# Performance work log

Measured on AMD Instinct MI355X. Metric: run time of the kernel, lower is better.

The kernel has to match this reference:

```python
import jax, jax.numpy as jnp
import numpy as np

NQ = 4
NL = 3
HEADS = 8

_H = jnp.asarray(np.array([[1, 1], [1, -1]], np.complex64) / np.sqrt(2.0))
_X = jnp.asarray(np.array([[0, 1], [1, 0]], np.complex64))
_Y = jnp.asarray(np.array([[0, -1j], [1j, 0]], np.complex64))
_Z = jnp.asarray(np.array([[1, 0], [0, -1]], np.complex64))
_CNOT = jnp.asarray(np.array([[1, 0, 0, 0], [0, 1, 0, 0], [0, 0, 0, 1], [0, 0, 1, 0]], np.complex64))


def _rx(t):
    c = jnp.cos(t / 2).astype(jnp.complex64)
    s = (-1j * jnp.sin(t / 2)).astype(jnp.complex64)
    return jnp.stack([jnp.stack([c, s]), jnp.stack([s, c])])


def _ry(t):
    c = jnp.cos(t / 2).astype(jnp.complex64)
    s = jnp.sin(t / 2).astype(jnp.complex64)
    return jnp.stack([jnp.stack([c, -s]), jnp.stack([s, c])])


def _rz(t):
    e = jnp.exp((-0.5j) * t).astype(jnp.complex64)
    z = jnp.zeros((), jnp.complex64)
    return jnp.stack([jnp.stack([e, z]), jnp.stack([z, jnp.conj(e)])])


def _crx(t):
    # control-RX in |control,target> basis
    return jnp.eye(4, dtype=jnp.complex64).at[2:, 2:].set(_rx(t))


def _ap1(psi, U, q):
    # apply 2x2 gate U on qubit axis q of psi:(2,2,2,2)
    return jnp.moveaxis(jnp.tensordot(U, psi, axes=[[1], [q]]), 0, q)


def _ap2(psi, U, q1, q2):
    p = jnp.moveaxis(psi, (q1, q2), (0, 1)).reshape(4, 4)
    p = (U @ p).reshape(2, 2, 2, 2)
    return jnp.moveaxis(p, (0, 1), (q1, q2))


def _expv(psi, P, q):
    return jnp.real(jnp.vdot(psi, _ap1(psi, P, q)))


def _circuit(inp, w, ew, gam, bet):
    # inp:(4,)  w,ew:(3,4)  gam,bet:(3,)  -> (12,) expvals Z,X,Y
    psi = jnp.zeros((16,), jnp.complex64).at[0].set(1.0).reshape(2, 2, 2, 2)
    for i in range(NQ):  # AngleEmbedding(rotation='Y')
        psi = _ap1(psi, _ry(inp[i]), i)
    for L in range(NL):
        for i in range(NQ):
            psi = _ap1(psi, _rx(w[L, i]), i)
            psi = _ap1(psi, _ry(w[L, i]), i)
            psi = _ap1(psi, _rz(w[L, i]), i)
        for i in range(NQ):  # CRX entangling ring
            psi = _ap2(psi, _crx(ew[L, i]), i, (i + 1) % NQ)
        # Grover diffusion
        for q in range(NQ):
            psi = _ap1(psi, _H, q)
        for q in range(NQ):
            psi = _ap1(psi, _X, q)
        psi = _ap1(psi, _H, NQ - 1)
        psi = psi.at[1, 1, 1, :].set(psi[1, 1, 1, ::-1])  # CCCX ctrl=[0,1,2] tgt=3
        psi = _ap1(psi, _H, NQ - 1)
        for q in range(NQ):
            psi = _ap1(psi, _X, q)
        for q in range(NQ):
            psi = _ap1(psi, _H, q)
        # QAOA cost + mixer
        for i in range(NQ - 1):
            psi = _ap2(psi, _CNOT, i, i + 1)
            psi = _ap1(psi, _rz(gam[L]), i + 1)
            psi = _ap2(psi, _CNOT, i, i + 1)
        for q in range(NQ):
            psi = _ap1(psi, _rx(bet[L]), q)
    meas = [_expv(psi, _Z, q) for q in range(NQ)]
    meas += [_expv(psi, _X, q) for q in range(NQ)]
    meas += [_expv(psi, _Y, q) for q in range(NQ)]
    return jnp.stack(meas)


_vqc = jax.vmap(_circuit, in_axes=(0, None, None, None, None))


def _layernorm(x, g, b, eps=1e-5):
    mu = jnp.mean(x, -1, keepdims=True)
    var = jnp.mean((x - mu) ** 2, -1, keepdims=True)
    return (x - mu) * jax.lax.rsqrt(var + eps) * g + b


def _qtransform(xf, Wp, bp, ln_g, ln_b, w, ew, gam, bet):
    p = jnp.tanh(xf @ Wp.T + bp)  # (BS,4)
    p = _layernorm(p, ln_g, ln_b)
    return _vqc(p, w, ew, gam, bet)  # (BS,12)


def setup_inputs() -> dict:
    key = jax.random.key(0)
    ks = jax.random.split(key, 32)
    B, S, Hd = 4, 1024, 512
    d = {"x": jax.random.normal(ks[0], (B, S, Hd), jnp.float32)}
    d["Wp"] = jax.random.normal(ks[1], (NQ, Hd), jnp.float32) * 0.05
    d["bp"] = jnp.zeros((NQ,), jnp.float32)
    d["ln_g"] = jnp.ones((NQ,), jnp.float32)
    d["ln_b"] = jnp.zeros((NQ,), jnp.float32)
    i = 2
    for pfx in ["q", "k", "v"]:
        d[pfx + "w"] = 0.01 * jax.random.normal(ks[i], (NL, NQ), jnp.float32)
        d[pfx + "e"] = 0.01 * jax.random.normal(ks[i + 1], (NL, NQ), jnp.float32)
        d[pfx + "g"] = 0.01 * jax.random.normal(ks[i + 2], (NL,), jnp.float32)
        d[pfx + "b"] = 0.01 * jax.random.normal(ks[i + 3], (NL,), jnp.float32)
        i += 4
    fused = 3 * NQ
    d["Wq"] = jax.random.normal(ks[i], (Hd, fused), jnp.float32) * 0.2
    d["bq"] = jnp.zeros((Hd,), jnp.float32)
    d["Wk"] = jax.random.normal(ks[i + 1], (Hd, fused), jnp.float32) * 0.2
    d["bk"] = jnp.zeros((Hd,), jnp.float32)
    d["Wv"] = jax.random.normal(ks[i + 2], (Hd, fused), jnp.float32) * 0.2
    d["bv"] = jnp.zeros((Hd,), jnp.float32)
    d["Wo"] = jax.random.normal(ks[i + 3], (Hd, Hd), jnp.float32) * 0.05
    d["bo"] = jnp.zeros((Hd,), jnp.float32)
    return d


def reference(x, Wp, bp, ln_g, ln_b, qw, qe, qg, qb, kw, ke, kg, kb, vw, ve, vg, vb,
              Wq, bq, Wk, bk, Wv, bv, Wo, bo):
    B, S, Hd = x.shape
    hd = Hd // HEADS
    xf = x.reshape(B * S, Hd)
    tq = _qtransform(xf, Wp, bp, ln_g, ln_b, qw, qe, qg, qb)
    tk = _qtransform(xf, Wp, bp, ln_g, ln_b, kw, ke, kg, kb)
    tv = _qtransform(xf, Wp, bp, ln_g, ln_b, vw, ve, vg, vb)
    q = (tq @ Wq.T + bq).reshape(B, S, HEADS, hd)
    k = (tk @ Wk.T + bk).reshape(B, S, HEADS, hd)
    v = (tv @ Wv.T + bv).reshape(B, S, HEADS, hd)
    scale = float(hd) ** 0.5
    attn = jax.nn.softmax(jnp.einsum('bqhd,bkhd->bhqk', q, k) / scale, axis=-1)
    out = jnp.einsum('bhqk,bkhd->bqhd', attn, v).reshape(B, S, Hd)
    return out @ Wo.T + bo
```

## Files before the change

### kernel.cpp

```cpp
#include <hip/hip_runtime.h>
#include <hip/hip_bf16.h>
#include <math.h>

#define NROWS 4096
#define HD 512
#define HEADS 8
#define HDD 64
#define SEQ 1024
#define QSCALE 0.18033688011112042f

typedef unsigned short u16;
typedef unsigned int u32;
typedef __attribute__((ext_vector_type(8))) short sh8;
typedef __attribute__((ext_vector_type(4))) float f4;

__device__ __forceinline__ f4 mfma16(sh8 a, sh8 b, f4 c) {
  return __builtin_amdgcn_mfma_f32_16x16x32_bf16(a, b, c, 0, 0, 0);
}

__device__ __forceinline__ u16 f2bf(float x) {
  union { float f; unsigned u; } v; v.f = x;
  unsigned r = v.u + 0x7fff + ((v.u >> 16) & 1);
  return (u16)(r >> 16);
}

#define SWZA(r, cb) ((((r) * 128) + (cb)) ^ (((r) & 7) << 4))
#define SWZB(r, cb) ((((r) * 256) + (cb)) ^ (((r) & 7) << 4))

__global__ __launch_bounds__(256) void k_prep(
    const float* __restrict__ qw, const float* __restrict__ qe,
    const float* __restrict__ qg, const float* __restrict__ qb,
    const float* __restrict__ kw, const float* __restrict__ ke,
    const float* __restrict__ kg, const float* __restrict__ kb,
    const float* __restrict__ vw, const float* __restrict__ ve,
    const float* __restrict__ vg, const float* __restrict__ vb,
    const float* __restrict__ Wq, const float* __restrict__ bq,
    const float* __restrict__ Wk, const float* __restrict__ bk,
    const float* __restrict__ Wv, const float* __restrict__ bv,
    float* __restrict__ Mout, u16* __restrict__ Wbout) {
  const int c = blockIdx.x;
  const int tid = threadIdx.x;

  if (c >= 3) {
    const int c2 = c - 3;
    const float* W = (c2 == 0) ? Wq : (c2 == 1) ? Wk : Wv;
    const float* bb = (c2 == 0) ? bq : (c2 == 1) ? bk : bv;
    const float sc = (c2 == 0) ? QSCALE : 1.f;
    for (int o = tid; o < 512; o += 256) {
      unsigned out[16];
#pragma unroll
      for (int i = 0; i < 16; ++i) out[i] = 0u;
      const float* wr = W + o * 12;
#pragma unroll
      for (int jp = 0; jp < 6; ++jp)
        out[jp] = (unsigned)f2bf(wr[2*jp] * sc) | ((unsigned)f2bf(wr[2*jp+1] * sc) << 16);
      out[6] = (unsigned)f2bf(bb[o] * sc);
      unsigned* dst = (unsigned*)(Wbout + (c2 * 512 + o) * 32);
#pragma unroll
      for (int i = 0; i < 16; ++i) dst[i] = out[i];
    }
    return;
  }

  __shared__ float aC[32], aS[32];
  __shared__ float GT[60][8];
  __shared__ int   GM[60][2];
  __shared__ float PF[3][16][2];
  __shared__ float SR[16][17], SI[16][17];
  __shared__ float TS[16], TI[16];
  __shared__ float Ur[256], Ui[256];

  const float* w = (c == 0) ? qw : (c == 1) ? kw : vw;
  const float* e = (c == 0) ? qe : (c == 1) ? ke : ve;
  const float* g = (c == 0) ? qg : (c == 1) ? kg : vg;
  const float* b = (c == 0) ? qb : (c == 1) ? kb : vb;

  if (tid < 30) {
    float ang = (tid < 12) ? w[tid] : (tid < 24) ? e[tid - 12]
               : (tid < 27) ? g[tid - 24] : b[tid - 27];
    float s_, c_;
    sincosf(0.5f * ang, &s_, &c_);
    aC[tid] = c_; aS[tid] = s_;
  }
  __syncthreads();

  if (tid < 60) {
    int L = tid / 20, s5 = tid % 20;
    int typ, aidx, M, C;
    if (s5 < 12) {
      int q = s5 / 3; typ = s5 % 3; aidx = L * 4 + q; M = 8 >> q; C = 0;
    } else if (s5 < 16) {
      int q = s5 - 12; typ = 0; aidx = 12 + L * 4 + q;
      C = 8 >> q; M = 8 >> ((q + 1) & 3);
    } else {
      int q = s5 - 16; typ = 0; aidx = 27 + L; M = 8 >> q; C = 0;
    }
    float cc = aC[aidx], ss = aS[aidx];
    float u0r = cc, u0i = 0.f, u1r = 0.f, u1i = 0.f,
          u2r = 0.f, u2i = 0.f, u3r = cc, u3i = 0.f;
    if (typ == 0)      { u1i = -ss; u2i = -ss; }
    else if (typ == 1) { u1r = -ss; u2r = ss; }
    else               { u0i = -ss; u3i = ss; }
    GT[tid][0] = u0r; GT[tid][1] = u0i; GT[tid][2] = u1r; GT[tid][3] = u1i;
    GT[tid][4] = u2r; GT[tid][5] = u2i; GT[tid][6] = u3r; GT[tid][7] = u3i;
    GM[tid][0] = M; GM[tid][1] = C;
  }
  if (tid >= 64 && tid < 112) {
    int idx = tid - 64, L = idx >> 4, a = idx & 15;
    float cg = aC[24 + L], sg = aS[24 + L];
    float c2 = cg * cg - sg * sg, s2 = 2.f * cg * sg;
    float c3 = cg * c2 - sg * s2, s3 = cg * s2 + sg * c2;
    int u = (a ^ (a >> 1)) & 7;
    int n = (u & 1) + ((u >> 1) & 1) + ((u >> 2) & 1);
    PF[L][a][0] = (n == 0 || n == 3) ? c3 : cg;
    PF[L][a][1] = (n == 0) ? -s3 : (n == 1) ? -sg : (n == 2) ? sg : s3;
  }
  for (int i = tid; i < 256; i += 256) {
    SR[i >> 4][i & 15] = (i >> 4) == (i & 15) ? 1.f : 0.f;
    SI[i >> 4][i & 15] = 0.f;
  }
  __syncthreads();

  const int p = tid >> 4, col = tid & 15;
  for (int L = 0; L < 3; ++L) {
    for (int s5 = 0; s5 < 16; ++s5) {
      if (tid < 128) {
        int gi = L * 20 + s5;
        const float* u = GT[gi];
        int M = GM[gi][0], C = GM[gi][1];
        int lo = p & (M - 1);
        int a = ((p - lo) << 1) | lo;
        int bb = a | M;
        bool act = (C == 0) | ((a & C) != 0);
        float ar = SR[a][col], ai = SI[a][col];
        float br = SR[bb][col], bi = SI[bb][col];
        float nar = u[0]*ar - u[1]*ai + u[2]*br - u[3]*bi;
        float nai = u[0]*ai + u[1]*ar + u[2]*bi + u[3]*br;
        float nbr = u[4]*ar - u[5]*ai + u[6]*br - u[7]*bi;
        float nbi = u[4]*ai + u[5]*ar + u[6]*bi + u[7]*br;
        SR[a][col]  = act ? nar : ar;  SI[a][col]  = act ? nai : ai;
        SR[bb][col] = act ? nbr : br;  SI[bb][col] = act ? nbi : bi;
      }
      __syncthreads();
    }
    if (tid < 16) {
      float sR = 0.f, sI = 0.f;
      for (int a = 0; a < 16; ++a) { sR += SR[a][tid]; sI += SI[a][tid]; }
      TS[tid] = sR * 0.125f; TI[tid] = sI * 0.125f;
    }
    __syncthreads();
    if (tid < 128) {
      for (int k = 0; k < 2; ++k) {
        int a = 2 * p + k;
        float vr = SR[a][col] - TS[col];
        float vi = SI[a][col] - TI[col];
        float pc = PF[L][a][0], ps = PF[L][a][1];
        SR[a][col] = vr * pc - vi * ps;
        SI[a][col] = vr * ps + vi * pc;
      }
    }
    __syncthreads();
    for (int s5 = 16; s5 < 20; ++s5) {
      if (tid < 128) {
        int gi = L * 20 + s5;
        const float* u = GT[gi];
        int M = GM[gi][0];
        int lo = p & (M - 1);
        int a = ((p - lo) << 1) | lo;
        int bb = a | M;
        float ar = SR[a][col], ai = SI[a][col];
        float br = SR[bb][col], bi = SI[bb][col];
        SR[a][col]  = u[0]*ar - u[1]*ai + u[2]*br - u[3]*bi;
        SI[a][col]  = u[0]*ai + u[1]*ar + u[2]*bi + u[3]*br;
        SR[bb][col] = u[4]*ar - u[5]*ai + u[6]*br - u[7]*bi;
        SI[bb][col] = u[4]*ai + u[5]*ar + u[6]*bi + u[7]*br;
      }
      __syncthreads();
    }
  }

  for (int i = tid; i < 256; i += 256) {
    Ur[i] = SR[i >> 4][i & 15];
    Ui[i] = SI[i >> 4][i & 15];
  }
  __syncthreads();

  if (tid < 192) {
    const int j = tid >> 4, a = tid & 15;
    const int typ = j >> 2;
    const int Mm = 8 >> (j & 3);
    float ax[4] = {0.f,0.f,0.f,0.f}, ay[4] = {0.f,0.f,0.f,0.f},
          az[4] = {0.f,0.f,0.f,0.f}, aw[4] = {0.f,0.f,0.f,0.f};
#pragma clang loop unroll_count(4)
    for (int k = 0; k < 16; ++k) {
      float uar = Ur[k * 16 + a], uai = Ui[k * 16 + a];
      int k2; float cR, cI;
      if (typ == 0)      { k2 = k;      float z = (k & Mm) ? -1.f : 1.f; cR = z*uar; cI = z*uai; }
      else if (typ == 1) { k2 = k ^ Mm; cR = uar; cI = uai; }
      else               { k2 = k ^ Mm; float sg = (k & Mm) ? 1.f : -1.f; cR = sg*uai; cI = -sg*uar; }
      const float* ur2 = Ur + k2 * 16;
      const float* ui2 = Ui + k2 * 16;
#pragma unroll
      for (int i = 0; i < 4; ++i) {
        ax[i] += cR * ur2[i*4+0] + cI * ui2[i*4+0];
        ay[i] += cR * ur2[i*4+1] + cI * ui2[i*4+1];
        az[i] += cR * ur2[i*4+2] + cI * ui2[i*4+2];
        aw[i] += cR * ur2[i*4+3] + cI * ui2[i*4+3];
      }
    }
    float* dst = Mout + ((c * 12 + j) * 16 + a) * 16;
#pragma unroll
    for (int i = 0; i < 4; ++i)
      ((float4*)dst)[i] = make_float4(ax[i], ay[i], az[i], aw[i]);
  }
}

__global__ __launch_bounds__(256) void k_fused(const float* __restrict__ x,
    const float* __restrict__ Wp, const float* __restrict__ bp,
    const float* __restrict__ ln_g, const float* __restrict__ ln_b,
    const float* __restrict__ Mg, const u16* __restrict__ Wb,
    u16* __restrict__ Qo, u16* __restrict__ Ko, u16* __restrict__ Vto) {
  const int rb = blockIdx.x;
  const int tid = threadIdx.x;
  __shared__ float Ml[3 * 12 * 256];
  __shared__ float pl[16][4];
  __shared__ float psil[16][17];
  __shared__ u16 tb[3 * 16 * 32];

  {
    const float4* src = (const float4*)Mg;
    for (int f = tid; f < 2304; f += 256) {
      int cj = f >> 6, e4 = f & 63;
      int j = cj % 12;
      ((float4*)Ml)[cj * 64 + (e4 ^ (j & 7))] = src[f];
    }
    for (int i = tid; i < 768; i += 256) ((u32*)tb)[i] = 0u;
    if (tid < 48) tb[(tid >> 4) * 512 + (tid & 15) * 32 + 12] = 0x3F80;
  }

  const int w = tid >> 6, lane = tid & 63;
  {
    float4 wpa[4], wpb[4];
#pragma unroll
    for (int j = 0; j < 4; ++j) {
      wpa[j] = *(const float4*)(Wp + j * HD + lane * 8);
      wpb[j] = *(const float4*)(Wp + j * HD + lane * 8 + 4);
    }
    for (int i = 0; i < 4; ++i) {
      int r = w * 4 + i;
      const float* xr = x + (rb * 16 + r) * HD + lane * 8;
      float4 xa = *(const float4*)xr, xb = *(const float4*)(xr + 4);
      float acc[4];
#pragma unroll
      for (int j = 0; j < 4; ++j)
        acc[j] = xa.x*wpa[j].x + xa.y*wpa[j].y + xa.z*wpa[j].z + xa.w*wpa[j].w
               + xb.x*wpb[j].x + xb.y*wpb[j].y + xb.z*wpb[j].z + xb.w*wpb[j].w;
#pragma unroll
      for (int j = 0; j < 4; ++j)
#pragma unroll
        for (int off = 32; off >= 1; off >>= 1)
          acc[j] += __shfl_xor(acc[j], off);
      if (lane == 0) {
        float v0 = tanhf(acc[0] + bp[0]);
        float v1 = tanhf(acc[1] + bp[1]);
        float v2 = tanhf(acc[2] + bp[2]);
        float v3 = tanhf(acc[3] + bp[3]);
        float mu = 0.25f * (v0 + v1 + v2 + v3);
        float d0 = v0 - mu, d1 = v1 - mu, d2 = v2 - mu, d3 = v3 - mu;
        float inv = rsqrtf(0.25f * (d0*d0 + d1*d1 + d2*d2 + d3*d3) + 1e-5f);
        pl[r][0] = d0 * inv * ln_g[0] + ln_b[0];
        pl[r][1] = d1 * inv * ln_g[1] + ln_b[1];
        pl[r][2] = d2 * inv * ln_g[2] + ln_b[2];
        pl[r][3] = d3 * inv * ln_g[3] + ln_b[3];
      }
    }
  }
  __syncthreads();

  if (tid < 16) {
    float cs[4], sn[4];
    sincosf(0.5f * pl[tid][0], &sn[0], &cs[0]);
    sincosf(0.5f * pl[tid][1], &sn[1], &cs[1]);
    sincosf(0.5f * pl[tid][2], &sn[2], &cs[2]);
    sincosf(0.5f * pl[tid][3], &sn[3], &cs[3]);
    float q01[4] = {cs[0]*cs[1], cs[0]*sn[1], sn[0]*cs[1], sn[0]*sn[1]};
    float q23[4] = {cs[2]*cs[3], cs[2]*sn[3], sn[2]*cs[3], sn[2]*sn[3]};
#pragma unroll
    for (int a = 0; a < 16; ++a) psil[tid][a] = q01[a >> 2] * q23[a & 3];
  }
  __syncthreads();

  if (tid < 192) {
    const int r = tid & 15, j = tid >> 4;
    float psi[16];
#pragma unroll
    for (int a = 0; a < 16; ++a) psi[a] = psil[r][a];
#pragma clang loop unroll(disable)
    for (int c = 0; c < 3; ++c) {
      const float4* Mj = (const float4*)(Ml + (c * 12 + j) * 256);
      float y = 0.f;
#pragma unroll
      for (int a = 0; a < 16; ++a) {
        float rsum = 0.f;
#pragma unroll
        for (int i = 0; i < 4; ++i) {
          float4 m4 = Mj[(a * 4 + i) ^ (j & 7)];
          rsum += m4.x*psi[i*4] + m4.y*psi[i*4+1] + m4.z*psi[i*4+2] + m4.w*psi[i*4+3];
        }
        y += psi[a] * rsum;
      }
      tb[c * 512 + r * 32 + j] = f2bf(y);
    }
  }
  __syncthreads();

  const int lr = lane & 15, lh = lane >> 4;
  const int b = rb >> 6, ss0 = (rb & 63) * 16;
  const f4 zero4 = (f4){0.f, 0.f, 0.f, 0.f};
#pragma unroll
  for (int c = 0; c < 3; ++c) {
    sh8 af = *(const sh8*)(tb + c * 512 + lr * 32 + lh * 8);
#pragma unroll
    for (int n = 0; n < 8; ++n) {
      int o = (w * 8 + n) * 16 + lr;
      sh8 bfr = *(const sh8*)(Wb + (c * 512 + o) * 32 + lh * 8);
      f4 acc = mfma16(af, bfr, zero4);
      if (c == 0) {
        int base = ((b * HEADS + (o >> 6)) * SEQ + ss0 + lh * 4) * HDD + (o & 63);
#pragma unroll
        for (int r = 0; r < 4; ++r) Qo[base + r * HDD] = f2bf(acc[r]);
      } else if (c == 1) {
        int base = ((b * HEADS + (o >> 6)) * SEQ + ss0 + lh * 4) * HDD + (o & 63);
#pragma unroll
        for (int r = 0; r < 4; ++r) Ko[base + r * HDD] = f2bf(acc[r]);
      } else {
        unsigned long long vv =
            (unsigned long long)((u32)f2bf(acc[0]) | ((u32)f2bf(acc[1]) << 16)) |
            ((unsigned long long)((u32)f2bf(acc[2]) | ((u32)f2bf(acc[3]) << 16)) << 32);
        *(unsigned long long*)(Vto + (b * 512 + o) * SEQ + ss0 + lh * 4) = vv;
      }
    }
  }
}

__global__ __launch_bounds__(256) void k_attn_mfma(const u16* __restrict__ Q,
    const u16* __restrict__ K, const u16* __restrict__ Vt,
    u16* __restrict__ Ob) {
  const int bh = blockIdx.y, qt = blockIdx.x;
  const int tid = threadIdx.x, w = tid >> 6, l = tid & 63;
  const int lr = l & 15, lh = l >> 4;

  __shared__ u16 Kl[2][128 * 64];
  __shared__ u16 Vl[2][64 * 128];
  __shared__ u16 Pl[4][16 * 128];

  const u16* Qb = Q + (bh * SEQ + qt * 64) * HDD;
  const u16* Kb = K + bh * SEQ * HDD;
  const u16* Vb = Vt + bh * HDD * SEQ;

  sh8 qf[2];
#pragma unroll
  for (int kk = 0; kk < 2; ++kk)
    qf[kk] = *(const sh8*)(Qb + (w * 16 + lr) * HDD + kk * 32 + lh * 8);

  f4 oacc[4];
  float lsum[4] = {0.f, 0.f, 0.f, 0.f};
#pragma unroll
  for (int n = 0; n < 4; ++n) oacc[n] = (f4){0.f, 0.f, 0.f, 0.f};

  sh8 kreg[4], vreg[4];

#define STAGE_LOAD(ch) { \
    _Pragma("unroll") \
    for (int i = 0; i < 4; ++i) { \
      int idx = i * 256 + tid; \
      kreg[i] = *(const sh8*)(Kb + ((ch) * 128 + (idx >> 3)) * HDD + (idx & 7) * 8); \
      vreg[i] = *(const sh8*)(Vb + (idx >> 4) * SEQ + (ch) * 128 + (idx & 15) * 8); \
    } }
#define STAGE_WRITE(buf) { \
    _Pragma("unroll") \
    for (int i = 0; i < 4; ++i) { \
      int idx = i * 256 + tid; \
      *(sh8*)((char*)Kl[buf] + SWZA(idx >> 3, (idx & 7) * 16)) = kreg[i]; \
      *(sh8*)((char*)Vl[buf] + SWZB(idx >> 4, (idx & 15) * 16)) = vreg[i]; \
    } }

  STAGE_LOAD(0)
  STAGE_WRITE(0)
  __syncthreads();

  for (int ch = 0; ch < SEQ / 128; ++ch) {
    const int cur = ch & 1;
    if (ch < 7) STAGE_LOAD(ch + 1)

    f4 sacc[8];
#pragma unroll
    for (int n = 0; n < 8; ++n) sacc[n] = (f4){0.f, 0.f, 0.f, 0.f};
#pragma unroll
    for (int kk = 0; kk < 2; ++kk) {
#pragma unroll
      for (int n = 0; n < 8; ++n) {
        sh8 kf = *(const sh8*)((const char*)Kl[cur] + SWZA(n * 16 + lr, kk * 64 + lh * 16));
        sacc[n] = mfma16(qf[kk], kf, sacc[n]);
      }
    }

#pragma unroll
    for (int n = 0; n < 8; ++n) {
#pragma unroll
      for (int r = 0; r < 4; ++r) {
        float pv = exp2f(sacc[n][r]);
        lsum[r] += pv;
        *(u16*)((char*)Pl[w] + SWZB(lh * 4 + r, (n * 16 + lr) * 2)) = f2bf(pv);
      }
    }

#pragma unroll
    for (int kk = 0; kk < 4; ++kk) {
      sh8 pf = *(const sh8*)((const char*)Pl[w] + SWZB(lr, kk * 64 + lh * 16));
#pragma unroll
      for (int n = 0; n < 4; ++n) {
        sh8 vf = *(const sh8*)((const char*)Vl[cur] + SWZB(n * 16 + lr, kk * 64 + lh * 16));
        oacc[n] = mfma16(pf, vf, oacc[n]);
      }
    }

    if (ch < 7) STAGE_WRITE(cur ^ 1)
    __syncthreads();
  }
#undef STAGE_LOAD
#undef STAGE_WRITE

#pragma unroll
  for (int r = 0; r < 4; ++r) {
    lsum[r] += __shfl_xor(lsum[r], 1); lsum[r] += __shfl_xor(lsum[r], 2);
    lsum[r] += __shfl_xor(lsum[r], 4); lsum[r] += __shfl_xor(lsum[r], 8);
  }

  int bb = bh >> 3, h = bh & 7;
#pragma unroll
  for (int r = 0; r < 4; ++r) {
    int row = qt * 64 + w * 16 + lh * 4 + r;
    float inv = 1.f / lsum[r];
#pragma unroll
    for (int n = 0; n < 4; ++n)
      Ob[(bb * SEQ + row) * HD + h * 64 + n * 16 + lr] = f2bf(oacc[n][r] * inv);
  }
}

__global__ __launch_bounds__(256) void k_oproj_mfma(const u16* __restrict__ A,
    const float* __restrict__ W, const float* __restrict__ bo,
    float* __restrict__ out) {
  const int nb = blockIdx.x, ob = blockIdx.y;
  const int tid = threadIdx.x, w = tid >> 6, l = tid & 63;
  const int lr = l & 15, lh = l >> 4;
  __shared__ u16 Al[64 * 64];
  __shared__ u16 Wl[64 * 64];
  f4 acc[4];
#pragma unroll
  for (int n = 0; n < 4; ++n) acc[n] = (f4){0.f, 0.f, 0.f, 0.f};
  for (int ch = 0; ch < 8; ++ch) {
    __syncthreads();
#pragma unroll
    for (int i = 0; i < 2; ++i) {
      int idx = i * 256 + tid;
      int r = idx >> 3, c8 = idx & 7;
      *(sh8*)((char*)Al + SWZA(r, c8 * 16)) =
          *(const sh8*)(A + (nb * 64 + r) * HD + ch * 64 + c8 * 8);
      const float* wp = W + (ob * 64 + r) * HD + ch * 64 + c8 * 8;
      float4 f0 = *(const float4*)wp;
      float4 f1 = *(const float4*)(wp + 4);
      sh8 wv;
      wv[0] = (short)f2bf(f0.x); wv[1] = (short)f2bf(f0.y);
      wv[2] = (short)f2bf(f0.z); wv[3] = (short)f2bf(f0.w);
      wv[4] = (short)f2bf(f1.x); wv[5] = (short)f2bf(f1.y);
      wv[6] = (short)f2bf(f1.z); wv[7] = (short)f2bf(f1.w);
      *(sh8*)((char*)Wl + SWZA(r, c8 * 16)) = wv;
    }
    __syncthreads();
#pragma unroll
    for (int kk = 0; kk < 2; ++kk) {
      sh8 af = *(const sh8*)((const char*)Al + SWZA(w * 16 + lr, kk * 64 + lh * 16));
#pragma unroll
      for (int n = 0; n < 4; ++n) {
        sh8 wf = *(const sh8*)((const char*)Wl + SWZA(n * 16 + lr, kk * 64 + lh * 16));
        acc[n] = mfma16(af, wf, acc[n]);
      }
    }
  }
#pragma unroll
  for (int r = 0; r < 4; ++r) {
    int row = nb * 64 + w * 16 + lh * 4 + r;
#pragma unroll
    for (int n = 0; n < 4; ++n) {
      int col = ob * 64 + n * 16 + lr;
      out[row * HD + col] = acc[n][r] + bo[col];
    }
  }
}

extern "C" void kernel_launch(void* const* d_in, const int* in_sizes, int n_in,
                              void* d_out, int out_size, void* d_ws, size_t ws_size,
                              hipStream_t stream) {
  const float* x    = (const float*)d_in[0];
  const float* Wp   = (const float*)d_in[1];
  const float* bp   = (const float*)d_in[2];
  const float* ln_g = (const float*)d_in[3];
  const float* ln_b = (const float*)d_in[4];
  const float* qw   = (const float*)d_in[5];
  const float* qe   = (const float*)d_in[6];
  const float* qg   = (const float*)d_in[7];
  const float* qb_  = (const float*)d_in[8];
  const float* kw   = (const float*)d_in[9];
  const float* ke   = (const float*)d_in[10];
  const float* kg   = (const float*)d_in[11];
  const float* kb_  = (const float*)d_in[12];
  const float* vw   = (const float*)d_in[13];
  const float* ve   = (const float*)d_in[14];
  const float* vg   = (const float*)d_in[15];
  const float* vb_  = (const float*)d_in[16];
  const float* Wq   = (const float*)d_in[17];
  const float* bq   = (const float*)d_in[18];
  const float* Wk   = (const float*)d_in[19];
  const float* bk   = (const float*)d_in[20];
  const float* Wv   = (const float*)d_in[21];
  const float* bv   = (const float*)d_in[22];
  const float* Wo   = (const float*)d_in[23];
  const float* bo   = (const float*)d_in[24];

  float* ws   = (float*)d_ws;
  float* Mbuf = ws;
  u16* Wbb = (u16*)(Mbuf + 9216);
  u16* qb  = Wbb + 49152;
  u16* kb  = qb + 32 * SEQ * HDD;
  u16* vtb = kb + 32 * SEQ * HDD;
  u16* ab  = vtb + 32 * SEQ * HDD;

  k_prep<<<6, 256, 0, stream>>>(qw, qe, qg, qb_, kw, ke, kg, kb_,
                                vw, ve, vg, vb_, Wq, bq, Wk, bk, Wv, bv,
                                Mbuf, Wbb);
  k_fused<<<NROWS / 16, 256, 0, stream>>>(x, Wp, bp, ln_g, ln_b, Mbuf, Wbb,
                                          qb, kb, vtb);
  dim3 ga(SEQ / 64, 32);
  k_attn_mfma<<<ga, 256, 0, stream>>>(qb, kb, vtb, ab);
  dim3 go(NROWS / 64, HD / 64);
  k_oproj_mfma<<<go, 256, 0, stream>>>(ab, Wo, bo, (float*)d_out);
}
```

Measured before the change: 84.80 us.

## Split fused QKV kernel into row-norm kernel and per-projection QKV kernel

```diff
diff --git a/kernel.cpp b/kernel.cpp
--- a/kernel.cpp
+++ b/kernel.cpp
@@ -215,74 +215,60 @@
   }
 }
 
-__global__ __launch_bounds__(256) void k_fused(const float* __restrict__ x,
+__global__ __launch_bounds__(256) void k_ln(const float* __restrict__ x,
     const float* __restrict__ Wp, const float* __restrict__ bp,
-    const float* __restrict__ ln_g, const float* __restrict__ ln_b,
+    const float* __restrict__ g, const float* __restrict__ b,
+    float* __restrict__ p) {
+  int row  = blockIdx.x * 4 + (threadIdx.x >> 6);
+  int lane = threadIdx.x & 63;
+  const float* xr = x + row * HD + lane * 8;
+  float4 xa = *(const float4*)xr;
+  float4 xb = *(const float4*)(xr + 4);
+  float acc[4];
+#pragma unroll
+  for (int j = 0; j < 4; ++j) {
+    const float* wr = Wp + j * HD + lane * 8;
+    float4 wa = *(const float4*)wr;
+    float4 wb = *(const float4*)(wr + 4);
+    acc[j] = xa.x*wa.x + xa.y*wa.y + xa.z*wa.z + xa.w*wa.w
+           + xb.x*wb.x + xb.y*wb.y + xb.z*wb.z + xb.w*wb.w;
+  }
+#pragma unroll
+  for (int j = 0; j < 4; ++j) {
+#pragma unroll
+    for (int off = 32; off >= 1; off >>= 1)
+      acc[j] += __shfl_xor(acc[j], off);
+  }
+  if (lane == 0) {
+    float v0 = tanhf(acc[0] + bp[0]);
+    float v1 = tanhf(acc[1] + bp[1]);
+    float v2 = tanhf(acc[2] + bp[2]);
+    float v3 = tanhf(acc[3] + bp[3]);
+    float mu = 0.25f * (v0 + v1 + v2 + v3);
+    float d0 = v0 - mu, d1 = v1 - mu, d2 = v2 - mu, d3 = v3 - mu;
+    float inv = rsqrtf(0.25f * (d0*d0 + d1*d1 + d2*d2 + d3*d3) + 1e-5f);
+    *(float4*)(p + row * 4) = make_float4(d0*inv*g[0] + b[0], d1*inv*g[1] + b[1],
+                                          d2*inv*g[2] + b[2], d3*inv*g[3] + b[3]);
+  }
+}
+
+__global__ __launch_bounds__(256) void k_qkv(const float* __restrict__ p,
     const float* __restrict__ Mg, const u16* __restrict__ Wb,
     u16* __restrict__ Qo, u16* __restrict__ Ko, u16* __restrict__ Vto) {
-  const int rb = blockIdx.x;
+  const int rb = blockIdx.x, c = blockIdx.y;
   const int tid = threadIdx.x;
-  __shared__ float Ml[3 * 12 * 256];
-  __shared__ float pl[16][4];
   __shared__ float psil[16][17];
-  __shared__ u16 tb[3 * 16 * 32];
-
-  {
-    const float4* src = (const float4*)Mg;
-    for (int f = tid; f < 2304; f += 256) {
-      int cj = f >> 6, e4 = f & 63;
-      int j = cj % 12;
-      ((float4*)Ml)[cj * 64 + (e4 ^ (j & 7))] = src[f];
-    }
-    for (int i = tid; i < 768; i += 256) ((u32*)tb)[i] = 0u;
-    if (tid < 48) tb[(tid >> 4) * 512 + (tid & 15) * 32 + 12] = 0x3F80;
-  }
-
-  const int w = tid >> 6, lane = tid & 63;
-  {
-    float4 wpa[4], wpb[4];
-#pragma unroll
-    for (int j = 0; j < 4; ++j) {
-      wpa[j] = *(const float4*)(Wp + j * HD + lane * 8);
-      wpb[j] = *(const float4*)(Wp + j * HD + lane * 8 + 4);
-    }
-    for (int i = 0; i < 4; ++i) {
-      int r = w * 4 + i;
-      const float* xr = x + (rb * 16 + r) * HD + lane * 8;
-      float4 xa = *(const float4*)xr, xb = *(const float4*)(xr + 4);
-      float acc[4];
-#pragma unroll
-      for (int j = 0; j < 4; ++j)
-        acc[j] = xa.x*wpa[j].x + xa.y*wpa[j].y + xa.z*wpa[j].z + xa.w*wpa[j].w
-               + xb.x*wpb[j].x + xb.y*wpb[j].y + xb.z*wpb[j].z + xb.w*wpb[j].w;
-#pragma unroll
-      for (int j = 0; j < 4; ++j)
-#pragma unroll
-        for (int off = 32; off >= 1; off >>= 1)
-          acc[j] += __shfl_xor(acc[j], off);
-      if (lane == 0) {
-        float v0 = tanhf(acc[0] + bp[0]);
-        float v1 = tanhf(acc[1] + bp[1]);
-        float v2 = tanhf(acc[2] + bp[2]);
-        float v3 = tanhf(acc[3] + bp[3]);
-        float mu = 0.25f * (v0 + v1 + v2 + v3);
-        float d0 = v0 - mu, d1 = v1 - mu, d2 = v2 - mu, d3 = v3 - mu;
-        float inv = rsqrtf(0.25f * (d0*d0 + d1*d1 + d2*d2 + d3*d3) + 1e-5f);
-        pl[r][0] = d0 * inv * ln_g[0] + ln_b[0];
-        pl[r][1] = d1 * inv * ln_g[1] + ln_b[1];
-        pl[r][2] = d2 * inv * ln_g[2] + ln_b[2];
-        pl[r][3] = d3 * inv * ln_g[3] + ln_b[3];
-      }
-    }
-  }
-  __syncthreads();
+  __shared__ u16 tb[16 * 32];
+
+  ((u32*)tb)[tid] = ((tid & 15) == 6) ? 0x3F80u : 0u;
 
   if (tid < 16) {
+    float4 in4 = *(const float4*)(p + (rb * 16 + tid) * 4);
     float cs[4], sn[4];
-    sincosf(0.5f * pl[tid][0], &sn[0], &cs[0]);
-    sincosf(0.5f * pl[tid][1], &sn[1], &cs[1]);
-    sincosf(0.5f * pl[tid][2], &sn[2], &cs[2]);
-    sincosf(0.5f * pl[tid][3], &sn[3], &cs[3]);
+    sincosf(0.5f * in4.x, &sn[0], &cs[0]);
+    sincosf(0.5f * in4.y, &sn[1], &cs[1]);
+    sincosf(0.5f * in4.z, &sn[2], &cs[2]);
+    sincosf(0.5f * in4.w, &sn[3], &cs[3]);
     float q01[4] = {cs[0]*cs[1], cs[0]*sn[1], sn[0]*cs[1], sn[0]*sn[1]};
     float q23[4] = {cs[2]*cs[3], cs[2]*sn[3], sn[2]*cs[3], sn[2]*sn[3]};
 #pragma unroll
@@ -295,50 +281,45 @@
     float psi[16];
 #pragma unroll
     for (int a = 0; a < 16; ++a) psi[a] = psil[r][a];
-#pragma clang loop unroll(disable)
-    for (int c = 0; c < 3; ++c) {
-      const float4* Mj = (const float4*)(Ml + (c * 12 + j) * 256);
-      float y = 0.f;
-#pragma unroll
-      for (int a = 0; a < 16; ++a) {
-        float rsum = 0.f;
-#pragma unroll
-        for (int i = 0; i < 4; ++i) {
-          float4 m4 = Mj[(a * 4 + i) ^ (j & 7)];
-          rsum += m4.x*psi[i*4] + m4.y*psi[i*4+1] + m4.z*psi[i*4+2] + m4.w*psi[i*4+3];
-        }
-        y += psi[a] * rsum;
-      }
-      tb[c * 512 + r * 32 + j] = f2bf(y);
-    }
+    const float4* Mj = (const float4*)(Mg + (c * 12 + j) * 256);
+    float y = 0.f;
+#pragma unroll
+    for (int a = 0; a < 16; ++a) {
+      float rsum = 0.f;
+#pragma unroll
+      for (int i = 0; i < 4; ++i) {
+        float4 m4 = Mj[a * 4 + i];
+        rsum += m4.x*psi[i*4] + m4.y*psi[i*4+1] + m4.z*psi[i*4+2] + m4.w*psi[i*4+3];
+      }
+      y += psi[a] * rsum;
+    }
+    tb[r * 32 + j] = f2bf(y);
   }
   __syncthreads();
 
+  const int w = tid >> 6, lane = tid & 63;
   const int lr = lane & 15, lh = lane >> 4;
   const int b = rb >> 6, ss0 = (rb & 63) * 16;
   const f4 zero4 = (f4){0.f, 0.f, 0.f, 0.f};
-#pragma unroll
-  for (int c = 0; c < 3; ++c) {
-    sh8 af = *(const sh8*)(tb + c * 512 + lr * 32 + lh * 8);
-#pragma unroll
-    for (int n = 0; n < 8; ++n) {
-      int o = (w * 8 + n) * 16 + lr;
-      sh8 bfr = *(const sh8*)(Wb + (c * 512 + o) * 32 + lh * 8);
-      f4 acc = mfma16(af, bfr, zero4);
-      if (c == 0) {
-        int base = ((b * HEADS + (o >> 6)) * SEQ + ss0 + lh * 4) * HDD + (o & 63);
-#pragma unroll
-        for (int r = 0; r < 4; ++r) Qo[base + r * HDD] = f2bf(acc[r]);
-      } else if (c == 1) {
-        int base = ((b * HEADS + (o >> 6)) * SEQ + ss0 + lh * 4) * HDD + (o & 63);
-#pragma unroll
-        for (int r = 0; r < 4; ++r) Ko[base + r * HDD] = f2bf(acc[r]);
-      } else {
-        unsigned long long vv =
-            (unsigned long long)((u32)f2bf(acc[0]) | ((u32)f2bf(acc[1]) << 16)) |
-            ((unsigned long long)((u32)f2bf(acc[2]) | ((u32)f2bf(acc[3]) << 16)) << 32);
-        *(unsigned long long*)(Vto + (b * 512 + o) * SEQ + ss0 + lh * 4) = vv;
-      }
+  sh8 af = *(const sh8*)(tb + lr * 32 + lh * 8);
+#pragma unroll
+  for (int n = 0; n < 8; ++n) {
+    int o = (w * 8 + n) * 16 + lr;
+    sh8 bfr = *(const sh8*)(Wb + (c * 512 + o) * 32 + lh * 8);
+    f4 acc = mfma16(af, bfr, zero4);
+    if (c == 0) {
+      int base = ((b * HEADS + (o >> 6)) * SEQ + ss0 + lh * 4) * HDD + (o & 63);
+#pragma unroll
+      for (int r = 0; r < 4; ++r) Qo[base + r * HDD] = f2bf(acc[r]);
+    } else if (c == 1) {
+      int base = ((b * HEADS + (o >> 6)) * SEQ + ss0 + lh * 4) * HDD + (o & 63);
+#pragma unroll
+      for (int r = 0; r < 4; ++r) Ko[base + r * HDD] = f2bf(acc[r]);
+    } else {
+      unsigned long long vv =
+          (unsigned long long)((u32)f2bf(acc[0]) | ((u32)f2bf(acc[1]) << 16)) |
+          ((unsigned long long)((u32)f2bf(acc[2]) | ((u32)f2bf(acc[3]) << 16)) << 32);
+      *(unsigned long long*)(Vto + (b * 512 + o) * SEQ + ss0 + lh * 4) = vv;
     }
   }
 }
@@ -530,7 +511,8 @@
 
   float* ws   = (float*)d_ws;
   float* Mbuf = ws;
-  u16* Wbb = (u16*)(Mbuf + 9216);
+  float* pbuf = Mbuf + 9216;
+  u16* Wbb = (u16*)(pbuf + 16384);
   u16* qb  = Wbb + 49152;
   u16* kb  = qb + 32 * SEQ * HDD;
   u16* vtb = kb + 32 * SEQ * HDD;
@@ -539,8 +521,9 @@
   k_prep<<<6, 256, 0, stream>>>(qw, qe, qg, qb_, kw, ke, kg, kb_,
                                 vw, ve, vg, vb_, Wq, bq, Wk, bk, Wv, bv,
                                 Mbuf, Wbb);
-  k_fused<<<NROWS / 16, 256, 0, stream>>>(x, Wp, bp, ln_g, ln_b, Mbuf, Wbb,
-                                          qb, kb, vtb);
+  k_ln<<<NROWS / 4, 256, 0, stream>>>(x, Wp, bp, ln_g, ln_b, pbuf);
+  dim3 gq(NROWS / 16, 3);
+  k_qkv<<<gq, 256, 0, stream>>>(pbuf, Mbuf, Wbb, qb, kb, vtb);
   dim3 ga(SEQ / 64, 32);
   k_attn_mfma<<<ga, 256, 0, stream>>>(qb, kb, vtb, ab);
   dim3 go(NROWS / 64, HD / 64);
```

Result: faster. 80.54 us (-5.0%).
